# Performance work log

Hardware: AMD Instinct MI355X
Metric: run time of the kernel (lower is better)

The kernel has to match this reference:

```python
import jax, jax.numpy as jnp
import numpy as np

N, E, IN, H, OUT = 100000, 600000, 128, 128, 64
BN_EPS = 1e-5


def setup_inputs() -> dict:
    key = jax.random.key(0)
    ks = jax.random.split(key, 8)
    def lin(k, i, o):
        return jax.random.normal(k, (i, o), jnp.float32) / np.float32(np.sqrt(i))
    return {
        "x": jax.random.normal(ks[0], (N, IN), jnp.float32),
        "edge_index": jax.random.randint(ks[1], (2, E), 0, N, dtype=jnp.int64),
        "W1": lin(ks[2], IN, H), "b1": jnp.zeros((H,), jnp.float32),
        "gamma": jnp.ones((H,), jnp.float32), "beta": jnp.zeros((H,), jnp.float32),
        "W2": lin(ks[3], H, H), "b2": jnp.zeros((H,), jnp.float32),
        "Wm1": lin(ks[4], H, H), "bm1": jnp.zeros((H,), jnp.float32),
        "Wm2": lin(ks[5], H, OUT), "bm2": jnp.zeros((OUT,), jnp.float32),
    }


def reference(x, edge_index, W1, b1, gamma, beta, W2, b2, Wm1, bm1, Wm2, bm2):
    # GINConv: h = MLP((1 + eps) * x + sum_{j in N(i)} x_j), eps = 0 (train_eps=False)
    src = edge_index[0]
    dst = edge_index[1]  # PyG aggregates messages at edge_index[1]
    agg = jax.ops.segment_sum(x[src], dst, num_segments=x.shape[0])  # [N, IN]
    h = agg + x
    # inner MLP: Linear -> BatchNorm (batch stats) -> ReLU -> Linear
    h = h @ W1 + b1
    mean = jnp.mean(h, axis=0)
    var = jnp.var(h, axis=0)
    h = (h - mean) * jax.lax.rsqrt(var + BN_EPS) * gamma + beta
    h = jax.nn.relu(h)
    h = h @ W2 + b2
    h = jax.nn.relu(h)  # .relu() after conv
    # output MLP (norm=None, dropout=0.5 -> identity at inference): Linear -> ReLU -> Linear
    h = jax.nn.relu(h @ Wm1 + bm1)
    return h @ Wm2 + bm2
```

## Files before the change

kernel.cpp:

```cpp
#include <hip/hip_runtime.h>
#include <hip/hip_bf16.h>
#include <stdint.h>

#define NNODES 100000
#define NEDGES 600000
#define SCAN_CHUNK 1024
#define SCAN_NB 98

typedef __attribute__((ext_vector_type(8))) short bf16x8;
typedef __attribute__((ext_vector_type(4))) float f32x4;
typedef __attribute__((ext_vector_type(4))) unsigned int u32x4;

__device__ inline float b2f(short b) {
    union { unsigned u; float f; } v;
    v.u = ((unsigned)(unsigned short)b) << 16;
    return v.f;
}
__device__ inline short f2b(float f) {
    union { float f; unsigned u; } v;
    v.f = f;
    unsigned r = (v.u + 0x7FFFu + ((v.u >> 16) & 1u)) >> 16;
    return (short)r;
}
__device__ inline unsigned packbf(float lo, float hi) {
    return ((unsigned)(unsigned short)f2b(hi) << 16) | (unsigned)(unsigned short)f2b(lo);
}
__device__ inline int swz(int row, int kbyte) {
    return (row * 256 + kbyte) ^ ((row & 7) << 4);
}
#define MFMA16(a, b, c) __builtin_amdgcn_mfma_f32_16x16x32_bf16(a, b, c, 0, 0, 0)

__device__ inline void stage_lds(const short* __restrict__ g, short* s, int w, int l, int n) {
#pragma unroll
    for (int i = 0; i < n; ++i) {
        int base = i * 4096 + w * 1024;
        __builtin_amdgcn_global_load_lds(
            (const __attribute__((address_space(1))) void*)((const char*)g + base + l * 16),
            (__attribute__((address_space(3))) void*)((char*)s + base), 16, 0, 0);
    }
}

__global__ __launch_bounds__(256) void k_prep(const float* __restrict__ x,
                                              const float* __restrict__ W1,
                                              const float* __restrict__ W2,
                                              const float* __restrict__ Wm1,
                                              const float* __restrict__ Wm2,
                                              short* __restrict__ xb, short* __restrict__ Wt,
                                              int* __restrict__ pos, float* __restrict__ stats) {
    int i = blockIdx.x * 256 + threadIdx.x;
    if (i < (NNODES + 1) * 16) {
        bf16x8 o = (bf16x8){0, 0, 0, 0, 0, 0, 0, 0};
        if (i < NNODES * 16) {
            const float4* p = (const float4*)(x + (size_t)i * 8);
            float4 a = p[0], b = p[1];
            o[0] = f2b(a.x); o[1] = f2b(a.y); o[2] = f2b(a.z); o[3] = f2b(a.w);
            o[4] = f2b(b.x); o[5] = f2b(b.y); o[6] = f2b(b.z); o[7] = f2b(b.w);
        }
        *(bf16x8*)(xb + (size_t)i * 8) = o;
    }
    if (i < NNODES) pos[i] = 0;
    if (i < 57344) {
        int jj, lane, kt, ct;
        const float* W;
        int ldw, off;
        if (i < 16384) { off = i; W = W1; ldw = 128; }
        else if (i < 32768) { off = i - 16384; W = W2; ldw = 128; }
        else if (i < 49152) { off = i - 32768; W = Wm1; ldw = 128; }
        else { off = i - 49152; W = Wm2; ldw = 64; }
        jj = off & 7;
        lane = (off >> 3) & 63;
        kt = (off >> 9) & 3;
        ct = (off >> 11) & 7;
        int lr = lane & 15, hi = lane >> 4;
        int c = ct * 16 + lr;
        int k = kt * 32 + hi * 8 + jj;
        Wt[i] = f2b(W[k * ldw + c]);
    }
    if (i < 256) stats[i] = 0.0f;
}


__global__ __launch_bounds__(256) void k_hist(const int* __restrict__ ei, int* __restrict__ cnt) {
    int e = blockIdx.x * 256 + threadIdx.x;
    if (e < NEDGES) atomicAdd(&cnt[ei[NEDGES + e]], 1);
}

__global__ __launch_bounds__(256) void k_scan1(const int* __restrict__ cnt, int* __restrict__ bsums) {
    __shared__ int sd[256];
    int b = blockIdx.x, t = threadIdx.x;
    int base = b * SCAN_CHUNK + t * 4;
    int s = 0;
#pragma unroll
    for (int i = 0; i < 4; ++i) {
        int idx = base + i;
        if (idx < NNODES) s += cnt[idx];
    }
    sd[t] = s;
    __syncthreads();
    for (int off = 128; off > 0; off >>= 1) {
        if (t < off) sd[t] += sd[t + off];
        __syncthreads();
    }
    if (t == 0) bsums[b] = sd[0];
}

__global__ __launch_bounds__(64) void k_scan2(int* __restrict__ bsums, int* __restrict__ rowptr) {
    if (threadIdx.x == 0 && blockIdx.x == 0) {
        int run = 0;
        for (int b = 0; b < SCAN_NB; ++b) {
            int v = bsums[b];
            bsums[b] = run;
            run += v;
        }
        rowptr[NNODES] = run;
    }
}

__global__ __launch_bounds__(256) void k_scan3(const int* __restrict__ cnt,
                                               const int* __restrict__ bsums,
                                               int* __restrict__ rowptr, int* __restrict__ pos) {
    __shared__ int sd[256];
    int b = blockIdx.x, t = threadIdx.x;
    int base = b * SCAN_CHUNK + t * 4;
    int v[4];
    int s = 0;
#pragma unroll
    for (int i = 0; i < 4; ++i) {
        int idx = base + i;
        v[i] = (idx < NNODES) ? cnt[idx] : 0;
        s += v[i];
    }
    sd[t] = s;
    __syncthreads();
    for (int off = 1; off < 256; off <<= 1) {
        int val = (t >= off) ? sd[t - off] : 0;
        __syncthreads();
        sd[t] += val;
        __syncthreads();
    }
    int run = sd[t] - s + bsums[b];
#pragma unroll
    for (int i = 0; i < 4; ++i) {
        int idx = base + i;
        if (idx < NNODES) {
            rowptr[idx] = run;
            pos[idx] = run;
            run += v[i];
        }
    }
}

__global__ __launch_bounds__(256) void k_fill(const int* __restrict__ ei, int* __restrict__ pos,
                                              int* __restrict__ elist) {
    int e = blockIdx.x * 256 + threadIdx.x;
    if (e >= NEDGES) return;
    int src = ei[e];
    int dst = ei[NEDGES + e];
    int p = atomicAdd(&pos[dst], 1);
    elist[p] = src;
}

__global__ __launch_bounds__(512, 8) void k_aggstats(const short* __restrict__ xb,
                                                     const int* __restrict__ rowptr,
                                                     const int* __restrict__ elist,
                                                     const short* __restrict__ W1pk,
                                                     short* __restrict__ bufb,
                                                     float* __restrict__ stats) {
    __shared__ __align__(16) short tile[64 * 128];
    __shared__ float Sred[2][2][128];

    int t = threadIdx.x, w = t >> 6, lane = t & 63;
    int sub = lane & 31, half = lane >> 5;
    int node0 = blockIdx.x * 64;
    const uint2* xr = (const uint2*)xb;

    int ridx = node0 + w * 8 + min(lane, 8);
    int vr = rowptr[min(ridx, NNODES)];

#pragma unroll
    for (int i = 0; i < 8; ++i) {
        int beg = __shfl(vr, i);
        int end = __shfl(vr, i + 1);
        int n = node0 + w * 8 + i;
        float a0 = 0.f, a1 = 0.f, a2 = 0.f, a3 = 0.f;
        if (n < NNODES) {
            int total = end - beg + 1;
            for (int base = 0; base < total; base += 64) {
                int j = base + lane;
                int ej = NNODES;
                if (j < total) ej = (j == 0) ? n : elist[beg + j - 1];
                int cnt = min(64, total - base);
                int pairs = (cnt + 1) >> 1;
                for (int ii = 0; ii < pairs; ii += 4) {
                    int j0 = 2 * ii + half;
                    int r0 = __shfl(ej, j0);
                    int r1 = __shfl(ej, j0 + 2);
                    int r2 = __shfl(ej, j0 + 4);
                    int r3 = __shfl(ej, j0 + 6);
                    uint2 v0 = xr[(size_t)r0 * 32 + sub];
                    uint2 v1 = xr[(size_t)r1 * 32 + sub];
                    uint2 v2 = xr[(size_t)r2 * 32 + sub];
                    uint2 v3 = xr[(size_t)r3 * 32 + sub];
                    a0 += b2f((short)(v0.x & 0xFFFF)) + b2f((short)(v1.x & 0xFFFF)) +
                          b2f((short)(v2.x & 0xFFFF)) + b2f((short)(v3.x & 0xFFFF));
                    a1 += b2f((short)(v0.x >> 16)) + b2f((short)(v1.x >> 16)) +
                          b2f((short)(v2.x >> 16)) + b2f((short)(v3.x >> 16));
                    a2 += b2f((short)(v0.y & 0xFFFF)) + b2f((short)(v1.y & 0xFFFF)) +
                          b2f((short)(v2.y & 0xFFFF)) + b2f((short)(v3.y & 0xFFFF));
                    a3 += b2f((short)(v0.y >> 16)) + b2f((short)(v1.y >> 16)) +
                          b2f((short)(v2.y >> 16)) + b2f((short)(v3.y >> 16));
                }
            }
        }
        a0 += __shfl_xor(a0, 32);
        a1 += __shfl_xor(a1, 32);
        a2 += __shfl_xor(a2, 32);
        a3 += __shfl_xor(a3, 32);
        if (half == 0) {
            int row = w * 8 + i;
            int b8 = sub * 8;
            int off = swz(row, b8 & ~15) + (b8 & 8);
            uint2 o;
            o.x = packbf(a0, a1);
            o.y = packbf(a2, a3);
            *(uint2*)((char*)tile + off) = o;
        }
    }
    __syncthreads();

    {
        int row = t >> 3, chunk = t & 7;
        int gr = node0 + row;
        if (gr < NNODES) {
            bf16x8 c0 = *(const bf16x8*)((char*)tile + swz(row, chunk * 32));
            bf16x8 c1 = *(const bf16x8*)((char*)tile + swz(row, chunk * 32 + 16));
            *(bf16x8*)(bufb + (size_t)gr * 128 + chunk * 16) = c0;
            *(bf16x8*)(bufb + (size_t)gr * 128 + chunk * 16 + 8) = c1;
        }
    }

    {
        int lr = lane & 15, hi = lane >> 4;
        int rg = w & 1, cg = w >> 1;
        f32x4 acc[2][2];
#pragma unroll
        for (int r = 0; r < 2; ++r)
#pragma unroll
            for (int c = 0; c < 2; ++c) acc[r][c] = (f32x4){0.f, 0.f, 0.f, 0.f};
#pragma unroll
        for (int kb = 0; kb < 4; ++kb) {
            int kbyte = kb * 64 + hi * 16;
            bf16x8 af[2], bw[2];
#pragma unroll
            for (int r = 0; r < 2; ++r)
                af[r] = *(const bf16x8*)((char*)tile + swz(rg * 32 + r * 16 + lr, kbyte));
#pragma unroll
            for (int c = 0; c < 2; ++c)
                bw[c] = *(const bf16x8*)(W1pk + (((cg * 2 + c) * 4 + kb) * 64 + lane) * 8);
#pragma unroll
            for (int r = 0; r < 2; ++r)
#pragma unroll
                for (int c = 0; c < 2; ++c) acc[r][c] = MFMA16(af[r], bw[c], acc[r][c]);
        }
        float s[2], q[2];
#pragma unroll
        for (int c = 0; c < 2; ++c) { s[c] = 0.f; q[c] = 0.f; }
#pragma unroll
        for (int c = 0; c < 2; ++c)
#pragma unroll
            for (int r = 0; r < 2; ++r)
#pragma unroll
                for (int rr = 0; rr < 4; ++rr) {
                    float v = acc[r][c][rr];
                    s[c] += v;
                    q[c] += v * v;
                }
#pragma unroll
        for (int c = 0; c < 2; ++c) {
            s[c] += __shfl_xor(s[c], 16); s[c] += __shfl_xor(s[c], 32);
            q[c] += __shfl_xor(q[c], 16); q[c] += __shfl_xor(q[c], 32);
        }
        if (lane < 16) {
#pragma unroll
            for (int c = 0; c < 2; ++c) {
                int col = (cg * 2 + c) * 16 + lane;
                Sred[0][rg][col] = s[c];
                Sred[1][rg][col] = q[c];
            }
        }
    }
    __syncthreads();
    if (t < 128) {
        atomicAdd(stats + t, Sred[0][0][t] + Sred[0][1][t]);
        atomicAdd(stats + 128 + t, Sred[1][0][t] + Sred[1][1][t]);
    }
}

__global__ __launch_bounds__(256, 4) void k_mlp(const short* __restrict__ bufb,
                                                const float* __restrict__ stats,
                                                const float* __restrict__ gamma,
                                                const float* __restrict__ beta,
                                                const short* __restrict__ Wt,
                                                const float* __restrict__ b2,
                                                const float* __restrict__ bm1,
                                                const float* __restrict__ bm2,
                                                float* __restrict__ out) {
    __shared__ __align__(16) short wbuf[16384];
    __shared__ float scl[3][128], shf[3][128], bm2s[64];

    int t = threadIdx.x, w = t >> 6, l = t & 63;
    int lr = l & 15, hi = l >> 4;
    size_t node0 = (size_t)blockIdx.x * 128 + w * 32;

    stage_lds(Wt, wbuf, w, l, 8);
    if (t < 128) {
        float mean = stats[t] * (1.0f / NNODES);
        float var = fmaxf(stats[128 + t] * (1.0f / NNODES) - mean * mean, 0.0f);
        float inv = rsqrtf(var + 1e-5f);
        float sc = gamma[t] * inv;
        scl[0][t] = sc;
        shf[0][t] = beta[t] - mean * sc;
        scl[1][t] = 1.0f;
        shf[1][t] = b2[t];
        scl[2][t] = 1.0f;
        shf[2][t] = bm1[t];
    }
    if (t < 64) bm2s[t] = bm2[t];

    bf16x8 bvA[4], bvB[4];
#pragma unroll
    for (int kt = 0; kt < 4; ++kt) {
        bvA[kt] = *(const bf16x8*)(bufb + (node0 + lr) * 128 + kt * 32 + hi * 8);
        bvB[kt] = *(const bf16x8*)(bufb + (node0 + 16 + lr) * 128 + kt * 32 + hi * 8);
    }
    __syncthreads();

    unsigned pwA[8][2], pwB[8][2];

    for (int g = 0; g < 3; ++g) {
#pragma unroll
        for (int ch = 0; ch < 2; ++ch) {
            f32x4 aA[4], aB[4];
#pragma unroll
            for (int cc = 0; cc < 4; ++cc) {
                aA[cc] = (f32x4){0.f, 0.f, 0.f, 0.f};
                aB[cc] = (f32x4){0.f, 0.f, 0.f, 0.f};
            }
#pragma unroll
            for (int kt = 0; kt < 4; ++kt) {
                bf16x8 wv[4];
#pragma unroll
                for (int cc = 0; cc < 4; ++cc)
                    wv[cc] = *(const bf16x8*)(wbuf + ((((ch * 4 + cc) * 4) + kt) * 64 + l) * 8);
#pragma unroll
                for (int cc = 0; cc < 4; ++cc) {
                    aA[cc] = MFMA16(wv[cc], bvA[kt], aA[cc]);
                    aB[cc] = MFMA16(wv[cc], bvB[kt], aB[cc]);
                }
            }
#pragma unroll
            for (int cc = 0; cc < 4; ++cc) {
                int ct = ch * 4 + cc;
                int c0 = ct * 16 + hi * 4;
                float4 s4 = *(const float4*)&scl[g][c0];
                float4 h4 = *(const float4*)&shf[g][c0];
                pwA[ct][0] = packbf(fmaxf(aA[cc][0] * s4.x + h4.x, 0.f),
                                    fmaxf(aA[cc][1] * s4.y + h4.y, 0.f));
                pwA[ct][1] = packbf(fmaxf(aA[cc][2] * s4.z + h4.z, 0.f),
                                    fmaxf(aA[cc][3] * s4.w + h4.w, 0.f));
                pwB[ct][0] = packbf(fmaxf(aB[cc][0] * s4.x + h4.x, 0.f),
                                    fmaxf(aB[cc][1] * s4.y + h4.y, 0.f));
                pwB[ct][1] = packbf(fmaxf(aB[cc][2] * s4.z + h4.z, 0.f),
                                    fmaxf(aB[cc][3] * s4.w + h4.w, 0.f));
            }
        }
        __syncthreads();
        if (g < 2) stage_lds(Wt + (g + 1) * 16384, wbuf, w, l, 8);
        else       stage_lds(Wt + 49152, wbuf, w, l, 4);

        {
            int h2 = hi >> 1, h1 = hi & 1;
#pragma unroll
            for (int kt = 0; kt < 4; ++kt) {
                unsigned nwA[4], nwB[4];
#pragma unroll
                for (int jp = 0; jp < 4; ++jp) {
                    int srcl = (2 * h1 + (jp >> 1)) * 16 + lr;
                    unsigned veA = (unsigned)__shfl((int)pwA[2 * kt][jp & 1], srcl);
                    unsigned voA = (unsigned)__shfl((int)pwA[2 * kt + 1][jp & 1], srcl);
                    unsigned veB = (unsigned)__shfl((int)pwB[2 * kt][jp & 1], srcl);
                    unsigned voB = (unsigned)__shfl((int)pwB[2 * kt + 1][jp & 1], srcl);
                    nwA[jp] = h2 ? voA : veA;
                    nwB[jp] = h2 ? voB : veB;
                }
                u32x4 uqA = (u32x4){nwA[0], nwA[1], nwA[2], nwA[3]};
                u32x4 uqB = (u32x4){nwB[0], nwB[1], nwB[2], nwB[3]};
                bvA[kt] = __builtin_bit_cast(bf16x8, uqA);
                bvB[kt] = __builtin_bit_cast(bf16x8, uqB);
            }
        }
        __syncthreads();
    }

#pragma unroll
    for (int ct = 0; ct < 4; ++ct) {
        f32x4 aA = (f32x4){0.f, 0.f, 0.f, 0.f};
        f32x4 aB = (f32x4){0.f, 0.f, 0.f, 0.f};
#pragma unroll
        for (int kt = 0; kt < 4; ++kt) {
            bf16x8 wv = *(const bf16x8*)(wbuf + ((ct * 4 + kt) * 64 + l) * 8);
            aA = MFMA16(bvA[kt], wv, aA);
            aB = MFMA16(bvB[kt], wv, aB);
        }
        float bias = bm2s[ct * 16 + lr];
#pragma unroll
        for (int rr = 0; rr < 4; ++rr) {
            size_t growA = node0 + hi * 4 + rr;
            size_t growB = node0 + 16 + hi * 4 + rr;
            if (growA < NNODES) out[growA * 64 + ct * 16 + lr] = aA[rr] + bias;
            if (growB < NNODES) out[growB * 64 + ct * 16 + lr] = aB[rr] + bias;
        }
    }
}

extern "C" void kernel_launch(void* const* d_in, const int* in_sizes, int n_in,
                              void* d_out, int out_size, void* d_ws, size_t ws_size,
                              hipStream_t stream) {
    const float* x     = (const float*)d_in[0];
    const int*   ei    = (const int*)d_in[1];
    const float* W1    = (const float*)d_in[2];
    const float* gamma = (const float*)d_in[4];
    const float* beta  = (const float*)d_in[5];
    const float* W2    = (const float*)d_in[6];
    const float* b2    = (const float*)d_in[7];
    const float* Wm1   = (const float*)d_in[8];
    const float* bm1   = (const float*)d_in[9];
    const float* Wm2   = (const float*)d_in[10];
    const float* bm2   = (const float*)d_in[11];
    float* out = (float*)d_out;

    char* ws = (char*)d_ws;
    short* xb    = (short*)ws;
    short* bufb  = xb + (size_t)(NNODES + 1) * 128;
    short* Wt    = bufb + (size_t)(NNODES + 128) * 128;
    float* stats = (float*)(Wt + 57344);
    int* rowptr  = (int*)(stats + 256);
    int* pos     = rowptr + (NNODES + 1);
    int* elist   = pos + NNODES;
    int* bsums   = elist + NEDGES;

    int gE = (NEDGES + 255) / 256;
    int gPrep = ((NNODES + 1) * 16 + 255) / 256;

    k_prep<<<gPrep, 256, 0, stream>>>(x, W1, W2, Wm1, Wm2, xb, Wt, pos, stats);
    k_hist<<<gE, 256, 0, stream>>>(ei, pos);
    k_scan1<<<SCAN_NB, 256, 0, stream>>>(pos, bsums);
    k_scan2<<<1, 64, 0, stream>>>(bsums, rowptr);
    k_scan3<<<SCAN_NB, 256, 0, stream>>>(pos, bsums, rowptr, pos);
    k_fill<<<gE, 256, 0, stream>>>(ei, pos, elist);

    int gAgg = (NNODES + 63) / 64;
    k_aggstats<<<gAgg, 512, 0, stream>>>(xb, rowptr, elist, Wt, bufb, stats);

    int nblkM = (NNODES + 127) / 128;
    k_mlp<<<nblkM, 256, 0, stream>>>(bufb, stats, gamma, beta, Wt, b2, bm1, bm2, out);
}
```

Before: 167.7 us.

## Batch neighbor gathers across 8 nodes per wave and shrink aggregation blocks

The aggregation kernel now preloads up to 128 edge indices per wave and issues gathers for all 8 nodes at once in chunks of 8 neighbors. This raises memory-level parallelism compared with handling one node at a time with short per-node loops. Blocks shrink to 32 nodes and 256 threads, and the BN statistics are written with per-wave global atomics instead of going through an LDS reduction. The trade-offs are higher register pressure from the 8x4 accumulators and 32 outstanding loads, wasted loads for padded slots when degrees are uneven, and twice as many stat atomics. The bf16 unpacking is also simplified into a helper.

```diff
diff --git a/kernel.cpp b/kernel.cpp
--- a/kernel.cpp
+++ b/kernel.cpp
@@ -24,6 +24,13 @@
 }
 __device__ inline unsigned packbf(float lo, float hi) {
     return ((unsigned)(unsigned short)f2b(hi) << 16) | (unsigned)(unsigned short)f2b(lo);
+}
+__device__ inline void accw(float& a, float& b, unsigned w) {
+    union { unsigned u; float f; } x, y;
+    x.u = w << 16;
+    y.u = w & 0xFFFF0000u;
+    a += x.f;
+    b += y.f;
 }
 __device__ inline int swz(int row, int kbyte) {
     return (row * 256 + kbyte) ^ ((row & 7) << 4);
@@ -160,69 +167,113 @@
     elist[p] = src;
 }
 
-__global__ __launch_bounds__(512, 8) void k_aggstats(const short* __restrict__ xb,
-                                                     const int* __restrict__ rowptr,
-                                                     const int* __restrict__ elist,
-                                                     const short* __restrict__ W1pk,
-                                                     short* __restrict__ bufb,
-                                                     float* __restrict__ stats) {
-    __shared__ __align__(16) short tile[64 * 128];
-    __shared__ float Sred[2][2][128];
+__global__ __launch_bounds__(256) void k_aggstats(const short* __restrict__ xb,
+                                                  const int* __restrict__ rowptr,
+                                                  const int* __restrict__ elist,
+                                                  const short* __restrict__ W1pk,
+                                                  short* __restrict__ bufb,
+                                                  float* __restrict__ stats) {
+    __shared__ __align__(16) short tile[32 * 128];
 
     int t = threadIdx.x, w = t >> 6, lane = t & 63;
     int sub = lane & 31, half = lane >> 5;
-    int node0 = blockIdx.x * 64;
+    int node0 = blockIdx.x * 32;
+    int nb = node0 + w * 8;
     const uint2* xr = (const uint2*)xb;
 
-    int ridx = node0 + w * 8 + min(lane, 8);
-    int vr = rowptr[min(ridx, NNODES)];
-
+    int vr = rowptr[min(nb + min(lane, 8), NNODES)];
+    int beg_all = __shfl(vr, 0);
+    int tot_e = __shfl(vr, 8) - beg_all;
+
+    int o_i[8], t_i[8];
+    int maxt = 0;
 #pragma unroll
     for (int i = 0; i < 8; ++i) {
         int beg = __shfl(vr, i);
         int end = __shfl(vr, i + 1);
-        int n = node0 + w * 8 + i;
-        float a0 = 0.f, a1 = 0.f, a2 = 0.f, a3 = 0.f;
-        if (n < NNODES) {
-            int total = end - beg + 1;
-            for (int base = 0; base < total; base += 64) {
-                int j = base + lane;
-                int ej = NNODES;
-                if (j < total) ej = (j == 0) ? n : elist[beg + j - 1];
-                int cnt = min(64, total - base);
-                int pairs = (cnt + 1) >> 1;
-                for (int ii = 0; ii < pairs; ii += 4) {
-                    int j0 = 2 * ii + half;
-                    int r0 = __shfl(ej, j0);
-                    int r1 = __shfl(ej, j0 + 2);
-                    int r2 = __shfl(ej, j0 + 4);
-                    int r3 = __shfl(ej, j0 + 6);
-                    uint2 v0 = xr[(size_t)r0 * 32 + sub];
-                    uint2 v1 = xr[(size_t)r1 * 32 + sub];
-                    uint2 v2 = xr[(size_t)r2 * 32 + sub];
-                    uint2 v3 = xr[(size_t)r3 * 32 + sub];
-                    a0 += b2f((short)(v0.x & 0xFFFF)) + b2f((short)(v1.x & 0xFFFF)) +
-                          b2f((short)(v2.x & 0xFFFF)) + b2f((short)(v3.x & 0xFFFF));
-                    a1 += b2f((short)(v0.x >> 16)) + b2f((short)(v1.x >> 16)) +
-                          b2f((short)(v2.x >> 16)) + b2f((short)(v3.x >> 16));
-                    a2 += b2f((short)(v0.y & 0xFFFF)) + b2f((short)(v1.y & 0xFFFF)) +
-                          b2f((short)(v2.y & 0xFFFF)) + b2f((short)(v3.y & 0xFFFF));
-                    a3 += b2f((short)(v0.y >> 16)) + b2f((short)(v1.y >> 16)) +
-                          b2f((short)(v2.y >> 16)) + b2f((short)(v3.y >> 16));
+        o_i[i] = beg - beg_all;
+        t_i[i] = end - beg + 1;
+        maxt = max(maxt, t_i[i]);
+    }
+
+    float acc[8][4];
+#pragma unroll
+    for (int i = 0; i < 8; ++i)
+#pragma unroll
+        for (int c = 0; c < 4; ++c) acc[i][c] = 0.0f;
+
+    if (tot_e <= 128) {
+        int ej0 = (lane < tot_e) ? elist[beg_all + lane] : NNODES;
+        int ej1 = (64 + lane < tot_e) ? elist[beg_all + 64 + lane] : NNODES;
+
+        for (int jb = 0; jb < maxt; jb += 8) {
+            uint2 v[8][4];
+#pragma unroll
+            for (int i = 0; i < 8; ++i) {
+#pragma unroll
+                for (int k = 0; k < 4; ++k) {
+                    int j = jb + 2 * k + half;
+                    int p = o_i[i] + j - 1;
+                    int s0 = __shfl(ej0, p & 63);
+                    int s1 = __shfl(ej1, p & 63);
+                    int src = (p < 64) ? s0 : s1;
+                    src = (j == 0) ? (nb + i) : src;
+                    src = (j < t_i[i] && nb + i < NNODES) ? src : NNODES;
+                    v[i][k] = xr[(size_t)src * 32 + sub];
                 }
             }
-        }
-        a0 += __shfl_xor(a0, 32);
-        a1 += __shfl_xor(a1, 32);
-        a2 += __shfl_xor(a2, 32);
-        a3 += __shfl_xor(a3, 32);
+#pragma unroll
+            for (int i = 0; i < 8; ++i)
+#pragma unroll
+                for (int k = 0; k < 4; ++k) {
+                    accw(acc[i][0], acc[i][1], v[i][k].x);
+                    accw(acc[i][2], acc[i][3], v[i][k].y);
+                }
+        }
+    } else {
+#pragma unroll
+        for (int i = 0; i < 8; ++i) {
+            int n = nb + i;
+            int total = t_i[i];
+            int beg = beg_all + o_i[i];
+            if (n < NNODES) {
+                for (int base = 0; base < total; base += 64) {
+                    int j = base + lane;
+                    int ej = NNODES;
+                    if (j < total) ej = (j == 0) ? n : elist[beg + j - 1];
+                    int cnt = min(64, total - base);
+                    int pairs = (cnt + 1) >> 1;
+                    for (int ii = 0; ii < pairs; ii += 4) {
+                        int j0 = 2 * ii + half;
+                        int r0 = __shfl(ej, j0);
+                        int r1 = __shfl(ej, j0 + 2);
+                        int r2 = __shfl(ej, j0 + 4);
+                        int r3 = __shfl(ej, j0 + 6);
+                        uint2 v0 = xr[(size_t)r0 * 32 + sub];
+                        uint2 v1 = xr[(size_t)r1 * 32 + sub];
+                        uint2 v2 = xr[(size_t)r2 * 32 + sub];
+                        uint2 v3 = xr[(size_t)r3 * 32 + sub];
+                        accw(acc[i][0], acc[i][1], v0.x); accw(acc[i][2], acc[i][3], v0.y);
+                        accw(acc[i][0], acc[i][1], v1.x); accw(acc[i][2], acc[i][3], v1.y);
+                        accw(acc[i][0], acc[i][1], v2.x); accw(acc[i][2], acc[i][3], v2.y);
+                        accw(acc[i][0], acc[i][1], v3.x); accw(acc[i][2], acc[i][3], v3.y);
+                    }
+                }
+            }
+        }
+    }
+
+#pragma unroll
+    for (int i = 0; i < 8; ++i) {
+#pragma unroll
+        for (int c = 0; c < 4; ++c) acc[i][c] += __shfl_xor(acc[i][c], 32);
         if (half == 0) {
             int row = w * 8 + i;
             int b8 = sub * 8;
             int off = swz(row, b8 & ~15) + (b8 & 8);
             uint2 o;
-            o.x = packbf(a0, a1);
-            o.y = packbf(a2, a3);
+            o.x = packbf(acc[i][0], acc[i][1]);
+            o.y = packbf(acc[i][2], acc[i][3]);
             *(uint2*)((char*)tile + off) = o;
         }
     }
@@ -241,26 +292,25 @@
 
     {
         int lr = lane & 15, hi = lane >> 4;
-        int rg = w & 1, cg = w >> 1;
-        f32x4 acc[2][2];
+        f32x4 a2[2][2];
 #pragma unroll
         for (int r = 0; r < 2; ++r)
 #pragma unroll
-            for (int c = 0; c < 2; ++c) acc[r][c] = (f32x4){0.f, 0.f, 0.f, 0.f};
+            for (int c = 0; c < 2; ++c) a2[r][c] = (f32x4){0.f, 0.f, 0.f, 0.f};
 #pragma unroll
         for (int kb = 0; kb < 4; ++kb) {
             int kbyte = kb * 64 + hi * 16;
             bf16x8 af[2], bw[2];
 #pragma unroll
             for (int r = 0; r < 2; ++r)
-                af[r] = *(const bf16x8*)((char*)tile + swz(rg * 32 + r * 16 + lr, kbyte));
+                af[r] = *(const bf16x8*)((char*)tile + swz(r * 16 + lr, kbyte));
 #pragma unroll
             for (int c = 0; c < 2; ++c)
-                bw[c] = *(const bf16x8*)(W1pk + (((cg * 2 + c) * 4 + kb) * 64 + lane) * 8);
+                bw[c] = *(const bf16x8*)(W1pk + (((w * 2 + c) * 4 + kb) * 64 + lane) * 8);
 #pragma unroll
             for (int r = 0; r < 2; ++r)
 #pragma unroll
-                for (int c = 0; c < 2; ++c) acc[r][c] = MFMA16(af[r], bw[c], acc[r][c]);
+                for (int c = 0; c < 2; ++c) a2[r][c] = MFMA16(af[r], bw[c], a2[r][c]);
         }
         float s[2], q[2];
 #pragma unroll
@@ -271,7 +321,7 @@
             for (int r = 0; r < 2; ++r)
 #pragma unroll
                 for (int rr = 0; rr < 4; ++rr) {
-                    float v = acc[r][c][rr];
+                    float v = a2[r][c][rr];
                     s[c] += v;
                     q[c] += v * v;
                 }
@@ -283,16 +333,11 @@
         if (lane < 16) {
 #pragma unroll
             for (int c = 0; c < 2; ++c) {
-                int col = (cg * 2 + c) * 16 + lane;
-                Sred[0][rg][col] = s[c];
-                Sred[1][rg][col] = q[c];
-            }
-        }
-    }
-    __syncthreads();
-    if (t < 128) {
-        atomicAdd(stats + t, Sred[0][0][t] + Sred[0][1][t]);
-        atomicAdd(stats + 128 + t, Sred[1][0][t] + Sred[1][1][t]);
+                int col = (w * 2 + c) * 16 + lane;
+                atomicAdd(stats + col, s[c]);
+                atomicAdd(stats + 128 + col, q[c]);
+            }
+        }
     }
 }
 
@@ -459,8 +504,8 @@
     k_scan3<<<SCAN_NB, 256, 0, stream>>>(pos, bsums, rowptr, pos);
     k_fill<<<gE, 256, 0, stream>>>(ei, pos, elist);
 
-    int gAgg = (NNODES + 63) / 64;
-    k_aggstats<<<gAgg, 512, 0, stream>>>(xb, rowptr, elist, Wt, bufb, stats);
+    int gAgg = (NNODES + 31) / 32;
+    k_aggstats<<<gAgg, 256, 0, stream>>>(xb, rowptr, elist, Wt, bufb, stats);
 
     int nblkM = (NNODES + 127) / 128;
     k_mlp<<<nblkM, 256, 0, stream>>>(bufb, stats, gamma, beta, Wt, b2, bm1, bm2, out);
```

After: 198.7 us. 18.5% more time.
